# Performance work log

Measured on AMD Instinct MI355X. Metric: run time of the kernel, lower is better.

Reference implementation:

```python
import jax, jax.numpy as jnp
import numpy as np

B, S, H = 2, 2048, 2048
NH, NKV, HD = 16, 4, 128
NEG = -1e9


def rotate_half(x):
    x1, x2 = x[..., : x.shape[-1] // 2], x[..., x.shape[-1] // 2 :]
    return jnp.concatenate((-x2, x1), axis=-1)


def setup_inputs() -> dict:
    key = jax.random.key(0)
    ks = jax.random.split(key, 6)
    hidden_states = jax.random.normal(ks[0], (B, S, H), dtype=jnp.float32)
    # causal additive mask [B, 1, S, S]
    causal = jnp.tril(jnp.ones((S, S), dtype=bool))
    attention_mask = jnp.where(causal, 0.0, NEG).astype(jnp.float32)
    attention_mask = jnp.broadcast_to(attention_mask, (B, 1, S, S))
    # rotary embeddings, base 10000
    inv_freq = 1.0 / (10000.0 ** (np.arange(0, HD, 2, dtype=np.float32) / HD))
    pos = np.arange(S, dtype=np.float32)
    freqs = np.outer(pos, inv_freq)  # [S, HD/2]
    emb = np.concatenate([freqs, freqs], axis=-1)  # [S, HD]
    cos = jnp.broadcast_to(jnp.asarray(np.cos(emb)), (B, S, HD))
    sin = jnp.broadcast_to(jnp.asarray(np.sin(emb)), (B, S, HD))
    sc = 0.02
    Wq = jax.random.normal(ks[1], (H, NH * HD), dtype=jnp.float32) * sc
    Wk = jax.random.normal(ks[2], (H, NKV * HD), dtype=jnp.float32) * sc
    Wv = jax.random.normal(ks[3], (H, NKV * HD), dtype=jnp.float32) * sc
    Wo = jax.random.normal(ks[4], (H, H), dtype=jnp.float32) * sc
    return {"hidden_states": hidden_states, "attention_mask": attention_mask,
            "cos": cos, "sin": sin, "Wq": Wq, "Wk": Wk, "Wv": Wv, "Wo": Wo}


def reference(hidden_states, attention_mask, cos, sin, Wq, Wk, Wv, Wo):
    b, s, _ = hidden_states.shape
    # projections -> [b, heads, s, hd]
    q = (hidden_states @ Wq).reshape(b, s, NH, HD).transpose(0, 2, 1, 3)
    k = (hidden_states @ Wk).reshape(b, s, NKV, HD).transpose(0, 2, 1, 3)
    v = (hidden_states @ Wv).reshape(b, s, NKV, HD).transpose(0, 2, 1, 3)
    # RoPE (cos/sin unsqueezed at dim 1)
    c, sn = cos[:, None], sin[:, None]
    q = q * c + rotate_half(q) * sn
    k = k * c + rotate_half(k) * sn
    # GQA repeat_kv: [b, nkv, s, hd] -> [b, nh, s, hd]
    n_rep = NH // NKV
    k = jnp.repeat(k, n_rep, axis=1)
    v = jnp.repeat(v, n_rep, axis=1)
    scores = jnp.einsum("bhqd,bhkd->bhqk", q, k) / jnp.sqrt(jnp.float32(HD))
    scores = scores + attention_mask
    probs = jax.nn.softmax(scores.astype(jnp.float32), axis=-1).astype(q.dtype)
    out = jnp.einsum("bhqk,bhkd->bhqd", probs, v)
    out = out.transpose(0, 2, 1, 3).reshape(b, s, NH * HD)
    return out @ Wo
```

## Files before the change

### kernel.cpp

```cpp
#include <hip/hip_runtime.h>
#include <hip/hip_bf16.h>

typedef __bf16 bf16;
typedef __bf16 bf16x4 __attribute__((ext_vector_type(4)));
typedef __bf16 bf16x8 __attribute__((ext_vector_type(8)));
typedef float f32x4 __attribute__((ext_vector_type(4)));

__device__ __forceinline__ void gload_lds16(const void* g, void* l) {
  __builtin_amdgcn_global_load_lds((__attribute__((address_space(1))) void*)(g),
                                   (__attribute__((address_space(3))) void*)(l), 16, 0, 0);
}
__device__ __forceinline__ float fexp2(float x) {
  float r;
  asm volatile("v_exp_f32 %0, %1" : "=v"(r) : "v"(x));
  return r;
}
#define S_WAITCNT_VM(n) asm volatile("s_waitcnt vmcnt(" #n ")" ::: "memory")

__global__ void k_diag(float* __restrict__ o, float v) { o[threadIdx.x] = v; }

__global__ void k_cvt_bf16(const float* __restrict__ x, bf16* __restrict__ y, int n4) {
  int i = blockIdx.x * blockDim.x + threadIdx.x;
  if (i < n4) {
    float4 v = reinterpret_cast<const float4*>(x)[i];
    bf16x4 o = {(bf16)v.x, (bf16)v.y, (bf16)v.z, (bf16)v.w};
    reinterpret_cast<bf16x4*>(y)[i] = o;
  }
}

__global__ void k_transpose_w(const float* __restrict__ W, bf16* __restrict__ Wt, int K, int N) {
  __shared__ float tile[32][33];
  int kb = blockIdx.x * 32, nb = blockIdx.y * 32;
  int tx = threadIdx.x & 31, ty = threadIdx.x >> 5;
#pragma unroll
  for (int i = 0; i < 32; i += 8)
    tile[ty + i][tx] = W[(size_t)(kb + ty + i) * N + nb + tx];
  __syncthreads();
#pragma unroll
  for (int i = 0; i < 32; i += 8)
    Wt[(size_t)(nb + ty + i) * K + kb + tx] = (bf16)tile[tx][ty + i];
}

__global__ void k_transpose_v(const bf16* __restrict__ Cq, bf16* __restrict__ Vt) {
  __shared__ bf16 tile[32][34];
  constexpr int S = 2048, CSTR = 3072;
  int sb = blockIdx.x * 32, db = blockIdx.y * 32, bh = blockIdx.z;
  int b = bh >> 2, kvh = bh & 3;
  int tx = threadIdx.x & 31, ty = threadIdx.x >> 5;
  const bf16* src = Cq + (size_t)b * S * CSTR + 2560 + kvh * 128;
#pragma unroll
  for (int i = 0; i < 32; i += 8)
    tile[ty + i][tx] = src[(size_t)(sb + ty + i) * CSTR + db + tx];
  __syncthreads();
  bf16* dst = Vt + (size_t)bh * 128 * S;
#pragma unroll
  for (int i = 0; i < 32; i += 8)
    dst[(size_t)(db + ty + i) * S + sb + tx] = tile[tx][ty + i];
}

template <typename OT>
__global__ __launch_bounds__(512) void k_gemm3(const bf16* __restrict__ A,
                                               const bf16* __restrict__ B0,
                                               const bf16* __restrict__ B1, int nsplit,
                                               OT* __restrict__ C, int Ncols, int Kd) {
  __shared__ __align__(16) bf16 lds_[65536];
  char* lds = (char*)lds_;
  const int t = threadIdx.x, w = t >> 6, l = t & 63;
  const int lr = l & 15, lk = l >> 4;
  const int gx = gridDim.x;
  const int flat = blockIdx.y * gx + blockIdx.x;
  const int xcd = flat & 7, local = flat >> 3;
  const int mi = (xcd & 3) * (gx >> 2) + (local & ((gx >> 2) - 1));
  const int ni = (xcd >> 2) * (gridDim.y >> 1) + (local >> 2);
  const int m0 = mi * 256, n0 = ni * 256;
  const int wm = w >> 2, wn = w & 3;
  const bf16* Bt = (n0 < nsplit) ? B0 + (size_t)n0 * Kd : B1 + (size_t)(n0 - nsplit) * Kd;
  const int nkt = Kd >> 6;
  const int srow = l >> 2;
  const int lch = (l & 3) ^ ((srow + (srow >> 2)) & 3);
  auto stA = [&](int tile, int unit) {
    if (tile >= nkt) return;
    const bf16* s = A + (size_t)(m0 + unit * 64 + (w >> 1) * 16 + srow) * Kd +
                    (tile << 6) + (w & 1) * 32 + lch * 8;
    gload_lds16(s, lds + (tile & 1) * 32768 + unit * 8192 + w * 1024);
  };
  auto stB = [&](int tile, int grp) {
    if (tile >= nkt) return;
    const bf16* s = Bt + (size_t)((w >> 1) * 64 + grp * 16 + srow) * Kd +
                    (tile << 6) + (w & 1) * 32 + lch * 8;
    gload_lds16(s, lds + 65536 + (tile & 1) * 32768 + grp * 8192 + w * 1024);
  };
  const int rdoff = lr * 64 + ((lk ^ ((lr + (lr >> 2)) & 3)) << 4);

  f32x4 acc[8][4] = {};
  stA(0, 0); stA(0, 1); stA(0, 2); stA(0, 3);
  stB(0, 0);
  stA(1, 0); stB(0, 1); stA(1, 1); stB(0, 2); stA(1, 2); stB(0, 3);

  for (int kt = 0; kt < nkt; ++kt) {
    const int buf = kt & 1;
    const char* Ab = lds + buf * 32768;
    const char* Bb = lds + 65536 + buf * 32768;
    bf16x8 af[8][2];
#pragma unroll
    for (int p = 0; p < 4; ++p) {
      if (kt + 1 < nkt) { S_WAITCNT_VM(6); } else { S_WAITCNT_VM(0); }
      __builtin_amdgcn_sched_barrier(0);
      __builtin_amdgcn_s_barrier();
      __builtin_amdgcn_sched_barrier(0);
      if (p == 0) stA(kt + 1, 3); else stA(kt + 2, p - 1);
      stB(kt + 1, p);
      if (p == 0) {
#pragma unroll
        for (int i = 0; i < 8; ++i) {
          const char* ub = Ab + (wm * 2 + (i >> 2)) * 8192 + (i & 3) * 2048;
          af[i][0] = *reinterpret_cast<const bf16x8*>(ub + rdoff);
          af[i][1] = *reinterpret_cast<const bf16x8*>(ub + 1024 + rdoff);
        }
      }
      bf16x8 b0 = *reinterpret_cast<const bf16x8*>(Bb + p * 8192 + wn * 2048 + rdoff);
      bf16x8 b1 = *reinterpret_cast<const bf16x8*>(Bb + p * 8192 + wn * 2048 + 1024 + rdoff);
      __builtin_amdgcn_s_setprio(1);
#pragma unroll
      for (int i = 0; i < 8; ++i) {
        acc[i][p] = __builtin_amdgcn_mfma_f32_16x16x32_bf16(af[i][0], b0, acc[i][p], 0, 0, 0);
        acc[i][p] = __builtin_amdgcn_mfma_f32_16x16x32_bf16(af[i][1], b1, acc[i][p], 0, 0, 0);
      }
      __builtin_amdgcn_s_setprio(0);
      __builtin_amdgcn_sched_barrier(0);
    }
  }
#pragma unroll
  for (int i = 0; i < 8; ++i)
#pragma unroll
    for (int j = 0; j < 4; ++j)
#pragma unroll
      for (int r = 0; r < 4; ++r) {
        int row = m0 + wm * 128 + i * 16 + lk * 4 + r;
        int col = n0 + wn * 64 + j * 16 + lr;
        if constexpr (sizeof(OT) == 4)
          C[(size_t)row * Ncols + col] = acc[i][j][r];
        else
          C[(size_t)row * Ncols + col] = (bf16)acc[i][j][r];
      }
}

template <int BM, typename OT>
__global__ __launch_bounds__(512) void k_gemm2(const bf16* __restrict__ A, const bf16* __restrict__ Bt,
                                               OT* __restrict__ C, int N, int Kd) {
  constexpr int NA = (BM / 16) * 2;
  constexpr int NB = 16;
  constexpr int NST = NA + NB;
  constexpr int NSW = NST / 8;
  constexpr int WM = BM / 4;
  constexpr int RG = WM / 16;
  __shared__ __align__(16) bf16 sAB[2][NST * 512];
  const int t = threadIdx.x, w = t >> 6, l = t & 63;
  const int lr = l & 15, lk = l >> 4;
  const int gx = gridDim.x;
  const int nwg = gx * gridDim.y;
  const int flat = blockIdx.y * gx + blockIdx.x;
  const int vid = (flat & 7) * (nwg >> 3) + (flat >> 3);
  const int m0 = (vid % gx) * BM, n0 = (vid / gx) * 128;
  const int wm = w >> 1, wn = w & 1;
  const int srow = l >> 2;
  const int lchunk = (l & 3) ^ (((l >> 5) & 1) << 1);
  const int rdoff = lr * 64 + ((lk * 16) ^ ((lr >> 3) << 5));
  const int nkt = Kd >> 6;
  char* lds = (char*)sAB;

  auto stage = [&](int kt, int buf) {
    const int k0 = kt << 6;
#pragma unroll
    for (int u = 0; u < NSW; ++u) {
      const int s = w * NSW + u;
      const bf16* src;
      if (s < NA)
        src = A + (size_t)(m0 + (s >> 1) * 16 + srow) * Kd + k0 + (s & 1) * 32 + lchunk * 8;
      else
        src = Bt + (size_t)(n0 + ((s - NA) >> 1) * 16 + srow) * Kd + k0 + ((s - NA) & 1) * 32 + lchunk * 8;
      gload_lds16(src, lds + buf * (NST * 1024) + s * 1024);
    }
  };

  f32x4 acc[RG][4] = {};
  stage(0, 0);
  stage(1, 1);
  if constexpr (NSW == 6) S_WAITCNT_VM(6); else S_WAITCNT_VM(4);
  __builtin_amdgcn_s_barrier();
  int c = 0;
  for (int kt = 0; kt < nkt; ++kt) {
    __builtin_amdgcn_sched_barrier(0);
    const char* base = lds + c * (NST * 1024);
    bf16x8 af[RG][2], bfr[4][2];
#pragma unroll
    for (int i = 0; i < RG; ++i)
#pragma unroll
      for (int kk = 0; kk < 2; ++kk)
        af[i][kk] = *reinterpret_cast<const bf16x8*>(base + ((wm * RG + i) * 2 + kk) * 1024 + rdoff);
#pragma unroll
    for (int j = 0; j < 4; ++j)
#pragma unroll
      for (int kk = 0; kk < 2; ++kk)
        bfr[j][kk] = *reinterpret_cast<const bf16x8*>(base + (NA + (wn * 4 + j) * 2 + kk) * 1024 + rdoff);
    __builtin_amdgcn_s_setprio(1);
#pragma unroll
    for (int i = 0; i < RG; ++i)
#pragma unroll
      for (int j = 0; j < 4; ++j) {
        acc[i][j] = __builtin_amdgcn_mfma_f32_16x16x32_bf16(af[i][0], bfr[j][0], acc[i][j], 0, 0, 0);
        acc[i][j] = __builtin_amdgcn_mfma_f32_16x16x32_bf16(af[i][1], bfr[j][1], acc[i][j], 0, 0, 0);
      }
    __builtin_amdgcn_s_setprio(0);
    __builtin_amdgcn_sched_barrier(0);
    asm volatile("" ::: "memory");
    __builtin_amdgcn_s_barrier();
    if (kt + 2 < nkt) stage(kt + 2, c);
    if (kt + 1 < nkt) {
      if (kt + 2 < nkt) {
        if constexpr (NSW == 6) S_WAITCNT_VM(6); else S_WAITCNT_VM(4);
      } else {
        S_WAITCNT_VM(0);
      }
      asm volatile("" ::: "memory");
      __builtin_amdgcn_s_barrier();
    }
    c ^= 1;
  }
#pragma unroll
  for (int i = 0; i < RG; ++i)
#pragma unroll
    for (int j = 0; j < 4; ++j)
#pragma unroll
      for (int r = 0; r < 4; ++r) {
        int row = m0 + wm * WM + i * 16 + lk * 4 + r;
        int col = n0 + wn * 64 + j * 16 + lr;
        if constexpr (sizeof(OT) == 4)
          C[(size_t)row * N + col] = acc[i][j][r];
        else
          C[(size_t)row * N + col] = (bf16)acc[i][j][r];
      }
}

__global__ void k_rope(bf16* __restrict__ X, const float* __restrict__ cs, const float* __restrict__ sn,
                       int nh, int rowstride, float scale, int total) {
  int idx = blockIdx.x * blockDim.x + threadIdx.x;
  if (idx >= total) return;
  int d = idx & 63;
  int th = idx >> 6;
  int h = th % nh;
  int tok = th / nh;
  size_t base = (size_t)tok * rowstride + h * 128;
  float c = cs[tok * 128 + d], s = sn[tok * 128 + d];
  float x1 = (float)X[base + d];
  float x2 = (float)X[base + d + 64];
  X[base + d] = (bf16)((x1 * c - x2 * s) * scale);
  X[base + d + 64] = (bf16)((x2 * c + x1 * s) * scale);
}

__global__ __launch_bounds__(512) void k_attn(const bf16* __restrict__ Q, const bf16* __restrict__ KV,
                                              const bf16* __restrict__ Vt, bf16* __restrict__ O) {
  constexpr int S = 2048, HD = 128, QSTR = 3072, OSTR = 2048;
  __shared__ __align__(16) char smem[81920];
  const int bid = blockIdx.x;
  const int vid = (bid & 7) * 32 + (bid >> 3);
  const int p = vid & 7, bh = vid >> 3;
  const int h = bh & 15, b = bh >> 4;
  const int t = threadIdx.x, w = t >> 6, l = t & 63;
  const int wq = w & 3, wk = w >> 2;
  const int lr = l & 15, lk = l >> 4;
  const int kvh = h >> 2;
  const int swz = (lr & 7) << 4;

  const char* kbase = (const char*)(KV + (size_t)b * S * QSTR + kvh * HD);
  const int krow_l = w * 8 + (l >> 4);
  const int kcol_l = (l & 15) << 4;
  const char* vtbase = (const char*)(Vt + (size_t)(b * 4 + kvh) * HD * S);
  const int vrow_l = w * 16 + (l >> 3);
  const int vcol_l = (l & 7) << 4;
  auto stage = [&](int kvb, int buf) {
#pragma unroll
    for (int c = 0; c < 2; ++c) {
      const int krow = krow_l + c * 4;
      gload_lds16(kbase + (size_t)(kvb + krow) * (QSTR * 2) + (kcol_l ^ ((krow & 7) << 4)),
                  smem + buf * 16384 + (w * 2 + c) * 1024);
      const int vrow = vrow_l + c * 8;
      gload_lds16(vtbase + (size_t)vrow * (S * 2) + kvb * 2 + (vcol_l ^ ((vrow & 7) << 4)),
                  smem + 32768 + buf * 16384 + (w * 2 + c) * 1024);
    }
  };
  char* sPb = smem + 65536 + w * 1280;

  for (int seg = 0; seg < 2; ++seg) {
    const int qtl = seg ? (15 - p) : p;
    const int qw = qtl * 128 + wq * 32;
    const int qlast = qw + 31;
    const int ntiles = (qtl + 1) * 2;
    int cur = 0;
    __syncthreads();
    stage(0, 0);
    bf16x8 qf[2][4];
#pragma unroll
    for (int rg = 0; rg < 2; ++rg) {
      const bf16* Qp = Q + (size_t)(b * S + qw + rg * 16 + lr) * QSTR + h * HD + lk * 8;
#pragma unroll
      for (int i = 0; i < 4; ++i) qf[rg][i] = *reinterpret_cast<const bf16x8*>(Qp + i * 32);
    }
    f32x4 oacc[2][8] = {};
    float mrow[2][4] = {{-1e30f, -1e30f, -1e30f, -1e30f}, {-1e30f, -1e30f, -1e30f, -1e30f}};
    float lsum[2][4] = {};
    __syncthreads();
    for (int tt = 0; tt < ntiles; ++tt) {
      const int kvb = tt * 64;
      if (tt + 1 < ntiles) stage(kvb + 64, cur ^ 1);
      const char* sKc = smem + cur * 16384;
      const char* sVc = smem + 32768 + cur * 16384;
      const int col0 = kvb + wk * 32;
      if (col0 <= qlast) {
        float pm[2][2][4];
#pragma unroll
        for (int c = 0; c < 2; ++c) {
          f32x4 s0 = {}, s1 = {};
#pragma unroll
          for (int kf = 0; kf < 4; ++kf) {
            bf16x8 kf8 = *reinterpret_cast<const bf16x8*>(
                sKc + (wk * 32 + c * 16 + lr) * 256 + (((kf * 64) + (lk << 4)) ^ swz));
            s0 = __builtin_amdgcn_mfma_f32_16x16x32_bf16(qf[0][kf], kf8, s0, 0, 0, 0);
            s1 = __builtin_amdgcn_mfma_f32_16x16x32_bf16(qf[1][kf], kf8, s1, 0, 0, 0);
          }
#pragma unroll
          for (int r = 0; r < 4; ++r) { pm[0][c][r] = s0[r]; pm[1][c][r] = s1[r]; }
        }
        if (col0 + 31 > qw) {
#pragma unroll
          for (int rg = 0; rg < 2; ++rg)
#pragma unroll
            for (int c = 0; c < 2; ++c) {
              const int col = col0 + c * 16 + lr;
#pragma unroll
              for (int r = 0; r < 4; ++r)
                if (col > qw + rg * 16 + lk * 4 + r) pm[rg][c][r] = -1e38f;
            }
        }
        float pmax[2][4];
#pragma unroll
        for (int rg = 0; rg < 2; ++rg)
#pragma unroll
          for (int r = 0; r < 4; ++r) pmax[rg][r] = fmaxf(pm[rg][0][r], pm[rg][1][r]);
        bool hi = false;
#pragma unroll
        for (int rg = 0; rg < 2; ++rg)
#pragma unroll
          for (int r = 0; r < 4; ++r) hi |= (pmax[rg][r] > mrow[rg][r] + 8.f);
        if (__any(hi)) {
          float mx[2][4];
#pragma unroll
          for (int rg = 0; rg < 2; ++rg)
#pragma unroll
            for (int r = 0; r < 4; ++r) mx[rg][r] = pmax[rg][r];
#pragma unroll
          for (int off = 1; off < 16; off <<= 1)
#pragma unroll
            for (int rg = 0; rg < 2; ++rg)
#pragma unroll
              for (int r = 0; r < 4; ++r) mx[rg][r] = fmaxf(mx[rg][r], __shfl_xor(mx[rg][r], off));
#pragma unroll
          for (int rg = 0; rg < 2; ++rg)
#pragma unroll
            for (int r = 0; r < 4; ++r) {
              float mn = fmaxf(mrow[rg][r], mx[rg][r]);
              float fac = fexp2(mrow[rg][r] - mn);
              mrow[rg][r] = mn;
              lsum[rg][r] *= fac;
#pragma unroll
              for (int ch = 0; ch < 8; ++ch) oacc[rg][ch][r] *= fac;
            }
        }
#pragma unroll
        for (int rg = 0; rg < 2; ++rg) {
#pragma unroll
          for (int c = 0; c < 2; ++c)
#pragma unroll
            for (int r = 0; r < 4; ++r) pm[rg][c][r] = fexp2(pm[rg][c][r] - mrow[rg][r]);
#pragma unroll
          for (int r = 0; r < 4; ++r) lsum[rg][r] += pm[rg][0][r] + pm[rg][1][r];
        }
        bf16x8 pf[2];
#pragma unroll
        for (int rg = 0; rg < 2; ++rg) {
#pragma unroll
          for (int c = 0; c < 2; ++c)
#pragma unroll
            for (int r = 0; r < 4; ++r)
              *(bf16*)(sPb + (lk * 4 + r) * 80 + (c * 16 + lr) * 2) = (bf16)pm[rg][c][r];
          pf[rg] = *reinterpret_cast<const bf16x8*>(sPb + lr * 80 + lk * 16);
        }
#pragma unroll
        for (int ch = 0; ch < 8; ++ch) {
          bf16x8 vf = *reinterpret_cast<const bf16x8*>(
              sVc + (ch * 16 + lr) * 128 + ((wk * 64 + (lk << 4)) ^ swz));
          oacc[0][ch] = __builtin_amdgcn_mfma_f32_16x16x32_bf16(pf[0], vf, oacc[0][ch], 0, 0, 0);
          oacc[1][ch] = __builtin_amdgcn_mfma_f32_16x16x32_bf16(pf[1], vf, oacc[1][ch], 0, 0, 0);
        }
      }
      __syncthreads();
      cur ^= 1;
    }
#pragma unroll
    for (int off = 1; off < 16; off <<= 1)
#pragma unroll
      for (int rg = 0; rg < 2; ++rg)
#pragma unroll
        for (int r = 0; r < 4; ++r) lsum[rg][r] += __shfl_xor(lsum[rg][r], off);
    float* ob = (float*)smem;
    float* mlb = (float*)(smem + 65536);
    if (wk == 1) {
#pragma unroll
      for (int rg = 0; rg < 2; ++rg) {
#pragma unroll
        for (int ch = 0; ch < 8; ++ch)
          *reinterpret_cast<f32x4*>(&ob[wq * 4096 + l * 64 + (rg * 8 + ch) * 4]) = oacc[rg][ch];
#pragma unroll
        for (int r = 0; r < 4; ++r) {
          mlb[wq * 1024 + l * 16 + rg * 8 + r] = mrow[rg][r];
          mlb[wq * 1024 + l * 16 + rg * 8 + 4 + r] = lsum[rg][r];
        }
      }
    }
    __syncthreads();
    if (wk == 0) {
      float sc0[2][4], sc1[2][4];
#pragma unroll
      for (int rg = 0; rg < 2; ++rg)
#pragma unroll
        for (int r = 0; r < 4; ++r) {
          float m1 = mlb[wq * 1024 + l * 16 + rg * 8 + r];
          float l1 = mlb[wq * 1024 + l * 16 + rg * 8 + 4 + r];
          float m = fmaxf(mrow[rg][r], m1);
          float w0 = fexp2(mrow[rg][r] - m), w1 = fexp2(m1 - m);
          float inv = 1.0f / (lsum[rg][r] * w0 + l1 * w1);
          sc0[rg][r] = w0 * inv;
          sc1[rg][r] = w1 * inv;
        }
#pragma unroll
      for (int rg = 0; rg < 2; ++rg) {
        bf16* Op = O + (size_t)(b * S + qw + rg * 16) * OSTR + h * HD;
#pragma unroll
        for (int ch = 0; ch < 8; ++ch) {
          f32x4 o1 = *reinterpret_cast<const f32x4*>(&ob[wq * 4096 + l * 64 + (rg * 8 + ch) * 4]);
#pragma unroll
          for (int r = 0; r < 4; ++r)
            Op[(size_t)(lk * 4 + r) * OSTR + ch * 16 + lr] =
                (bf16)(oacc[rg][ch][r] * sc0[rg][r] + o1[r] * sc1[rg][r]);
        }
      }
    }
  }
}

extern "C" void kernel_launch(void* const* d_in, const int* in_sizes, int n_in,
                              void* d_out, int out_size, void* d_ws, size_t ws_size,
                              hipStream_t stream) {
  const float* hs = (const float*)d_in[0];
  const float* cosb = (const float*)d_in[2];
  const float* sinb = (const float*)d_in[3];
  const float* Wq = (const float*)d_in[4];
  const float* Wk = (const float*)d_in[5];
  const float* Wv = (const float*)d_in[6];
  const float* Wo = (const float*)d_in[7];
  float* out = (float*)d_out;

  constexpr int B = 2, S = 2048, H = 2048, NH = 16, NKV = 4, HD = 128;
  constexpr int T = B * S;
  constexpr size_t MB = 1024 * 1024;

  const size_t ws_need = 24 * MB;
  if (ws_size < ws_need) {
    k_diag<<<1, 64, 0, stream>>>(out, 1000.0f + (float)(ws_size / MB));
    return;
  }
  bf16* Xb = (bf16*)d_ws;
  bf16* WtQ = (bf16*)((char*)d_ws + 16 * MB);
  bf16* Ob = Xb;
  bf16* Cqkv = (bf16*)d_out;
  bf16* Vtb = (bf16*)((char*)d_out + 24 * MB);
  bf16* WtKV = (bf16*)((char*)d_out + 28 * MB);

  k_cvt_bf16<<<T * H / 4 / 256, 256, 0, stream>>>(hs, Xb, T * H / 4);

  k_transpose_w<<<dim3(H / 32, H / 32), 256, 0, stream>>>(Wq, WtQ, H, H);
  k_transpose_w<<<dim3(H / 32, (NKV * HD) / 32), 256, 0, stream>>>(Wk, WtKV, H, NKV * HD);
  k_transpose_w<<<dim3(H / 32, (NKV * HD) / 32), 256, 0, stream>>>(Wv, WtKV + (size_t)(NKV * HD) * H, H, NKV * HD);

  k_gemm3<bf16><<<dim3(16, 12), 512, 0, stream>>>(Xb, WtQ, WtKV, 2048, Cqkv, 3072, H);

  k_transpose_v<<<dim3(S / 32, HD / 32, B * NKV), 256, 0, stream>>>(Cqkv, Vtb);

  const float qscale = 0.12751743f;
  k_rope<<<(T * NH * 64) / 256, 256, 0, stream>>>(Cqkv, cosb, sinb, NH, 3072, qscale, T * NH * 64);
  k_rope<<<(T * NKV * 64) / 256, 256, 0, stream>>>(Cqkv + 2048, cosb, sinb, NKV, 3072, 1.0f, T * NKV * 64);

  k_attn<<<256, 512, 0, stream>>>(Cqkv, Cqkv + 2048, Vtb, Ob);

  k_transpose_w<<<dim3(H / 32, H / 32), 256, 0, stream>>>(Wo, WtQ, H, H);
  k_gemm2<256, float><<<dim3(16, 16), 512, 0, stream>>>(Ob, WtQ, out, H, H);
}
```

Measured before the change: 224.9 us.

## Restructure QKV GEMM mainloop with row-major swizzled LDS tiles

New measurement: 213.3 us. 5.2% less time.

```diff
diff --git a/kernel.cpp b/kernel.cpp
--- a/kernel.cpp
+++ b/kernel.cpp
@@ -16,6 +16,7 @@
   return r;
 }
 #define S_WAITCNT_VM(n) asm volatile("s_waitcnt vmcnt(" #n ")" ::: "memory")
+#define LDS_FENCE() asm volatile("" ::: "memory")
 
 __global__ void k_diag(float* __restrict__ o, float v) { o[threadIdx.x] = v; }
 
@@ -59,12 +60,11 @@
 }
 
 template <typename OT>
-__global__ __launch_bounds__(512) void k_gemm3(const bf16* __restrict__ A,
+__global__ __launch_bounds__(512) void k_gemm4(const bf16* __restrict__ A,
                                                const bf16* __restrict__ B0,
                                                const bf16* __restrict__ B1, int nsplit,
                                                OT* __restrict__ C, int Ncols, int Kd) {
-  __shared__ __align__(16) bf16 lds_[65536];
-  char* lds = (char*)lds_;
+  __shared__ __align__(16) char lds[131072];
   const int t = threadIdx.x, w = t >> 6, l = t & 63;
   const int lr = l & 15, lk = l >> 4;
   const int gx = gridDim.x;
@@ -76,58 +76,55 @@
   const int wm = w >> 2, wn = w & 3;
   const bf16* Bt = (n0 < nsplit) ? B0 + (size_t)n0 * Kd : B1 + (size_t)(n0 - nsplit) * Kd;
   const int nkt = Kd >> 6;
-  const int srow = l >> 2;
-  const int lch = (l & 3) ^ ((srow + (srow >> 2)) & 3);
-  auto stA = [&](int tile, int unit) {
-    if (tile >= nkt) return;
-    const bf16* s = A + (size_t)(m0 + unit * 64 + (w >> 1) * 16 + srow) * Kd +
-                    (tile << 6) + (w & 1) * 32 + lch * 8;
-    gload_lds16(s, lds + (tile & 1) * 32768 + unit * 8192 + w * 1024);
+  const int srow8 = l >> 3;
+  const int sk = ((l & 7) ^ srow8) * 8;
+  auto stA = [&](int kt, int g) {
+    if (kt >= nkt) return;
+    const bf16* s = A + (size_t)(m0 + w * 32 + g * 8 + srow8) * Kd + (kt << 6) + sk;
+    gload_lds16(s, lds + (kt & 1) * 32768 + (w * 32 + g * 8) * 128);
   };
-  auto stB = [&](int tile, int grp) {
-    if (tile >= nkt) return;
-    const bf16* s = Bt + (size_t)((w >> 1) * 64 + grp * 16 + srow) * Kd +
-                    (tile << 6) + (w & 1) * 32 + lch * 8;
-    gload_lds16(s, lds + 65536 + (tile & 1) * 32768 + grp * 8192 + w * 1024);
+  auto stB = [&](int kt, int g) {
+    if (kt >= nkt) return;
+    const bf16* s = Bt + (size_t)(w * 32 + g * 8 + srow8) * Kd + (kt << 6) + sk;
+    gload_lds16(s, lds + 65536 + (kt & 1) * 32768 + (w * 32 + g * 8) * 128);
   };
-  const int rdoff = lr * 64 + ((lk ^ ((lr + (lr >> 2)) & 3)) << 4);
 
   f32x4 acc[8][4] = {};
-  stA(0, 0); stA(0, 1); stA(0, 2); stA(0, 3);
-  stB(0, 0);
-  stA(1, 0); stB(0, 1); stA(1, 1); stB(0, 2); stA(1, 2); stB(0, 3);
+#pragma unroll
+  for (int g = 0; g < 4; ++g) { stA(0, g); stB(0, g); }
 
   for (int kt = 0; kt < nkt; ++kt) {
-    const int buf = kt & 1;
-    const char* Ab = lds + buf * 32768;
-    const char* Bb = lds + 65536 + buf * 32768;
-    bf16x8 af[8][2];
-#pragma unroll
-    for (int p = 0; p < 4; ++p) {
-      if (kt + 1 < nkt) { S_WAITCNT_VM(6); } else { S_WAITCNT_VM(0); }
-      __builtin_amdgcn_sched_barrier(0);
-      __builtin_amdgcn_s_barrier();
-      __builtin_amdgcn_sched_barrier(0);
-      if (p == 0) stA(kt + 1, 3); else stA(kt + 2, p - 1);
-      stB(kt + 1, p);
-      if (p == 0) {
-#pragma unroll
-        for (int i = 0; i < 8; ++i) {
-          const char* ub = Ab + (wm * 2 + (i >> 2)) * 8192 + (i & 3) * 2048;
-          af[i][0] = *reinterpret_cast<const bf16x8*>(ub + rdoff);
-          af[i][1] = *reinterpret_cast<const bf16x8*>(ub + 1024 + rdoff);
-        }
-      }
-      bf16x8 b0 = *reinterpret_cast<const bf16x8*>(Bb + p * 8192 + wn * 2048 + rdoff);
-      bf16x8 b1 = *reinterpret_cast<const bf16x8*>(Bb + p * 8192 + wn * 2048 + 1024 + rdoff);
-      __builtin_amdgcn_s_setprio(1);
-#pragma unroll
-      for (int i = 0; i < 8; ++i) {
-        acc[i][p] = __builtin_amdgcn_mfma_f32_16x16x32_bf16(af[i][0], b0, acc[i][p], 0, 0, 0);
-        acc[i][p] = __builtin_amdgcn_mfma_f32_16x16x32_bf16(af[i][1], b1, acc[i][p], 0, 0, 0);
-      }
-      __builtin_amdgcn_s_setprio(0);
-      __builtin_amdgcn_sched_barrier(0);
+    const char* Ab = lds + (kt & 1) * 32768;
+    const char* Bb = lds + 65536 + (kt & 1) * 32768;
+    bf16x8 bfr[4];
+#pragma unroll
+    for (int kk = 0; kk < 2; ++kk) {
+#pragma unroll
+      for (int h = 0; h < 2; ++h) {
+        if (kk == 0 && h == 0) { S_WAITCNT_VM(0); }
+        __builtin_amdgcn_s_barrier();
+        LDS_FENCE();
+        const int ph = kk * 2 + h;
+        stA(kt + 1, ph);
+        stB(kt + 1, ph);
+        const int rc = ((kk * 4 + lk) ^ (lr & 7)) << 4;
+        bf16x8 af[4];
+#pragma unroll
+        for (int i = 0; i < 4; ++i)
+          af[i] = *reinterpret_cast<const bf16x8*>(Ab + (wm * 128 + (h * 4 + i) * 16 + lr) * 128 + rc);
+        if (h == 0) {
+#pragma unroll
+          for (int j = 0; j < 4; ++j)
+            bfr[j] = *reinterpret_cast<const bf16x8*>(Bb + (wn * 64 + j * 16 + lr) * 128 + rc);
+        }
+        __builtin_amdgcn_s_setprio(1);
+#pragma unroll
+        for (int i = 0; i < 4; ++i)
+#pragma unroll
+          for (int j = 0; j < 4; ++j)
+            acc[h * 4 + i][j] = __builtin_amdgcn_mfma_f32_16x16x32_bf16(af[i], bfr[j], acc[h * 4 + i][j], 0, 0, 0);
+        __builtin_amdgcn_s_setprio(0);
+      }
     }
   }
 #pragma unroll
@@ -492,7 +489,7 @@
   k_transpose_w<<<dim3(H / 32, (NKV * HD) / 32), 256, 0, stream>>>(Wk, WtKV, H, NKV * HD);
   k_transpose_w<<<dim3(H / 32, (NKV * HD) / 32), 256, 0, stream>>>(Wv, WtKV + (size_t)(NKV * HD) * H, H, NKV * HD);
 
-  k_gemm3<bf16><<<dim3(16, 12), 512, 0, stream>>>(Xb, WtQ, WtKV, 2048, Cqkv, 3072, H);
+  k_gemm4<bf16><<<dim3(16, 12), 512, 0, stream>>>(Xb, WtQ, WtKV, 2048, Cqkv, 3072, H);
 
   k_transpose_v<<<dim3(S / 32, HD / 32, B * NKV), 256, 0, stream>>>(Cqkv, Vtb);
 
```
